# Optimization experiments

Hardware: AMD Instinct MI355X
Metric: run time of the kernel (lower is better)

## Reference

```python
import jax, jax.numpy as jnp
import numpy as np

NUM_GROUPS = 4
EPS = 1e-6


def group_norm(x, scale, bias):
    # x: [b, c, h, w]; GroupNorm32 computes stats in fp32 (x already fp32 here)
    b, c, h, w = x.shape
    xg = x.reshape(b, NUM_GROUPS, c // NUM_GROUPS, h, w)
    mean = jnp.mean(xg, axis=(2, 3, 4), keepdims=True)
    var = jnp.var(xg, axis=(2, 3, 4), keepdims=True)
    xn = ((xg - mean) * jax.lax.rsqrt(var + EPS)).reshape(b, c, h, w)
    return xn * scale[None, :, None, None] + bias[None, :, None, None]


def conv1x1(x, w, b):
    # 1x1 conv == channel mix: x [b,c,h,w], w [co,ci]
    return jnp.einsum('bchw,dc->bdhw', x, w) + b[None, :, None, None]


def setup_inputs() -> dict:
    key = jax.random.key(0)
    ks = jax.random.split(key, 6)
    c = 256
    s = 1.0 / np.sqrt(c)
    return {
        'x': jax.random.normal(ks[0], (4, c, 64, 64), dtype=jnp.float32),
        'gn_scale': jnp.ones((c,), jnp.float32),
        'gn_bias': jnp.zeros((c,), jnp.float32),
        'wq': jax.random.normal(ks[1], (c, c), jnp.float32) * s,
        'bq': jnp.zeros((c,), jnp.float32),
        'wk': jax.random.normal(ks[2], (c, c), jnp.float32) * s,
        'bk': jnp.zeros((c,), jnp.float32),
        'wv': jax.random.normal(ks[3], (c, c), jnp.float32) * s,
        'bv': jnp.zeros((c,), jnp.float32),
        'wproj': jax.random.normal(ks[4], (c, c), jnp.float32) * s,
        'bproj': jnp.zeros((c,), jnp.float32),
    }


def reference(x, gn_scale, gn_bias, wq, bq, wk, bk, wv, bv, wproj, bproj):
    b, c, h, w = x.shape
    hw = h * w
    h_ = group_norm(x, gn_scale, gn_bias)
    q = conv1x1(h_, wq, bq).reshape(b, c, hw)  # [b, c, hw]
    k = conv1x1(h_, wk, bk).reshape(b, c, hw)
    v = conv1x1(h_, wv, bv).reshape(b, c, hw)
    scale = jnp.float32(1.0 / np.sqrt(c))
    # attn[b, i, j] = sum_c q[b,c,i] * k[b,c,j], fp32 softmax over j
    attn = jnp.einsum('bci,bcj->bij', q.astype(jnp.float32), k.astype(jnp.float32)) * scale
    attn = jax.nn.softmax(attn, axis=-1).astype(x.dtype)
    # out[b, c, i] = sum_j v[b,c,j] * attn[b,i,j]
    out = jnp.einsum('bcj,bij->bci', v, attn).reshape(b, c, h, w)
    out = conv1x1(out, wproj, bproj)
    return x + out
```

## Files before the change

### kernel.cpp

```cpp
#include <hip/hip_runtime.h>


#define HW 4096
#define CCH 256
#define NBATCH 4
#define GN_N (64 * HW)

typedef unsigned short u16;
typedef __attribute__((ext_vector_type(8))) short bf16x8;
typedef __attribute__((ext_vector_type(4))) float f32x4;
typedef __attribute__((ext_vector_type(4))) u16 u16x4;

__device__ __forceinline__ u16 f2bf(float f) {
  unsigned u = __float_as_uint(f);
  u += 0x7fffu + ((u >> 16) & 1u);
  return (u16)(u >> 16);
}
__device__ __forceinline__ float bf2f(u16 h) { return __uint_as_float(((unsigned)h) << 16); }

__device__ __forceinline__ void gload_lds16(const void* g, void* l) {
  __builtin_amdgcn_global_load_lds(
      (const __attribute__((address_space(1))) unsigned*)g,
      (__attribute__((address_space(3))) unsigned*)l, 16, 0, 0);
}

__global__ __launch_bounds__(256) void gn_partial(const float* __restrict__ x,
                                                  float* __restrict__ part) {
  const int bg = blockIdx.y, blk = blockIdx.x, tid = threadIdx.x;
  const float4* X = (const float4*)(x + (size_t)bg * GN_N);
  float s = 0.f, ss = 0.f;
#pragma unroll
  for (int u = 0; u < 8; ++u) {
    float4 v = X[blk * 2048 + u * 256 + tid];
    s += v.x + v.y + v.z + v.w;
    ss += v.x * v.x + v.y * v.y + v.z * v.z + v.w * v.w;
  }
  for (int off = 32; off; off >>= 1) { s += __shfl_xor(s, off); ss += __shfl_xor(ss, off); }
  __shared__ float rs[4], rss[4];
  const int w = tid >> 6;
  if ((tid & 63) == 0) { rs[w] = s; rss[w] = ss; }
  __syncthreads();
  if (tid == 0) {
    part[(bg * 32 + blk) * 2 + 0] = rs[0] + rs[1] + rs[2] + rs[3];
    part[(bg * 32 + blk) * 2 + 1] = rss[0] + rss[1] + rss[2] + rss[3];
  }
}

__global__ void gn_finalize(const float* __restrict__ part, float2* __restrict__ stats) {
  const int t = threadIdx.x;
  if (t < 16) {
    float s = 0.f, ss = 0.f;
    for (int u = 0; u < 32; ++u) { s += part[(t * 32 + u) * 2]; ss += part[(t * 32 + u) * 2 + 1]; }
    const float mean = s * (1.0f / GN_N);
    const float var = ss * (1.0f / GN_N) - mean * mean;
    stats[t] = make_float2(mean, rsqrtf(var + 1e-6f));
  }
}

__global__ __launch_bounds__(256) void norm_tr(const float* __restrict__ x,
                                               const float2* __restrict__ stats,
                                               const float* __restrict__ gsc,
                                               const float* __restrict__ gbi,
                                               u16* __restrict__ Ht) {
  __shared__ u16 T[64][72];
  const int i0 = blockIdx.x * 64, c0 = blockIdx.y * 64, b = blockIdx.z;
  const int tid = threadIdx.x;
  const int cl = tid >> 4;
  const int il4 = (tid & 15) * 4;
#pragma unroll
  for (int it = 0; it < 4; ++it) {
    const int c = c0 + it * 16 + cl;
    const float2 st = stats[b * 4 + (c >> 6)];
    const float sc = gsc[c] * st.y;
    const float bi = gbi[c] - st.x * sc;
    const float4 v = *(const float4*)&x[((size_t)(b * CCH + c)) * HW + i0 + il4];
    T[il4 + 0][it * 16 + cl] = f2bf(v.x * sc + bi);
    T[il4 + 1][it * 16 + cl] = f2bf(v.y * sc + bi);
    T[il4 + 2][it * 16 + cl] = f2bf(v.z * sc + bi);
    T[il4 + 3][it * 16 + cl] = f2bf(v.w * sc + bi);
  }
  __syncthreads();
  const int il = tid >> 2, cs = (tid & 3) * 16;
  const uint4 a = *(const uint4*)&T[il][cs];
  const uint4 b2 = *(const uint4*)&T[il][cs + 8];
  const size_t o = ((size_t)b * HW + i0 + il) * CCH + c0 + cs;
  *(uint4*)&Ht[o] = a;
  *(uint4*)&Ht[o + 8] = b2;
}

__global__ __launch_bounds__(256) void wcast(const float* __restrict__ w0, const float* __restrict__ w1,
                                             const float* __restrict__ w2, const float* __restrict__ w3,
                                             u16* __restrict__ dst) {
  const float* src = blockIdx.y == 0 ? w0 : blockIdx.y == 1 ? w1 : blockIdx.y == 2 ? w2 : w3;
  u16* d = dst + (size_t)blockIdx.y * 65536;
  const int idx = (blockIdx.x * 256 + threadIdx.x) * 8;
  const float4 a = *(const float4*)&src[idx];
  const float4 c = *(const float4*)&src[idx + 4];
  uint4 p;
  p.x = (unsigned)f2bf(a.x) | ((unsigned)f2bf(a.y) << 16);
  p.y = (unsigned)f2bf(a.z) | ((unsigned)f2bf(a.w) << 16);
  p.z = (unsigned)f2bf(c.x) | ((unsigned)f2bf(c.y) << 16);
  p.w = (unsigned)f2bf(c.z) | ((unsigned)f2bf(c.w) << 16);
  *(uint4*)&d[idx] = p;
}

template <int EPI, bool HASB>
__global__ __launch_bounds__(256) void gemm2(
    const u16* __restrict__ A, int lda, long sA,
    const u16* __restrict__ Bm, int ldb, long sB,
    void* __restrict__ O0, int ldo, long sO,
    void* __restrict__ O1, void* __restrict__ O2,
    const float* __restrict__ b0, const float* __restrict__ b1, const float* __restrict__ b2,
    const float* __restrict__ aux, long sAux,
    float scale, int K) {
  __shared__ char lsA[32768], lsB[32768];
  int bx, by, bz;
  {
    const int nx = gridDim.x, ny = gridDim.y;
    const int lin = blockIdx.x + nx * (blockIdx.y + ny * blockIdx.z);
    const int q = (nx * ny * (int)gridDim.z) >> 3;
    const int wg = (lin & 7) * q + (lin >> 3);
    bx = wg % nx; const int t2 = wg / nx; by = t2 % ny; bz = t2 / ny;
  }
  const int tid = threadIdx.x;
  const int w = tid >> 6, l = tid & 63;
  const int wm = w >> 1, wn = w & 1;
  const int m0 = by * 128, n0 = bx * 128;
  const u16* Ab = A + (size_t)bz * sA;
  const u16* Bb = Bm + (size_t)bz * sB;

  f32x4 acc[4][4];
#pragma unroll
  for (int i = 0; i < 4; ++i)
#pragma unroll
    for (int j = 0; j < 4; ++j)
#pragma unroll
      for (int q2 = 0; q2 < 4; ++q2) acc[i][j][q2] = 0.f;

  auto stage = [&](int buf, int k0) {
#pragma unroll
    for (int s = 0; s < 4; ++s) {
      const int o = s * 4096 + tid * 16;
      const int r = o >> 7;
      const int c = ((o >> 4) & 7) ^ (r & 7);
      const int ke = c * 8;
      gload_lds16(Ab + (size_t)(m0 + r) * lda + k0 + ke, lsA + buf * 16384 + s * 4096 + w * 1024);
      gload_lds16(Bb + (size_t)(n0 + r) * ldb + k0 + ke, lsB + buf * 16384 + s * 4096 + w * 1024);
    }
  };

  const int nt = K >> 6;
  stage(0, 0);
  asm volatile("s_waitcnt vmcnt(0)" ::: "memory");
  __syncthreads();
  for (int t = 0; t < nt; ++t) {
    const int cur = t & 1;
    if (t + 1 < nt) stage(cur ^ 1, (t + 1) << 6);
#pragma unroll
    for (int kk = 0; kk < 2; ++kk) {
      bf16x8 aF[4], bF[4];
#pragma unroll
      for (int mi = 0; mi < 4; ++mi) {
        const int r = wm * 64 + mi * 16 + (l & 15);
        const int cc = (kk * 4 + (l >> 4)) ^ (r & 7);
        aF[mi] = *(const bf16x8*)(lsA + cur * 16384 + r * 128 + cc * 16);
      }
#pragma unroll
      for (int ni = 0; ni < 4; ++ni) {
        const int r = wn * 64 + ni * 16 + (l & 15);
        const int cc = (kk * 4 + (l >> 4)) ^ (r & 7);
        bF[ni] = *(const bf16x8*)(lsB + cur * 16384 + r * 128 + cc * 16);
      }
#pragma unroll
      for (int mi = 0; mi < 4; ++mi)
#pragma unroll
        for (int ni = 0; ni < 4; ++ni)
          acc[mi][ni] = __builtin_amdgcn_mfma_f32_16x16x32_bf16(aF[mi], bF[ni], acc[mi][ni], 0, 0, 0);
    }
    asm volatile("s_waitcnt vmcnt(0)" ::: "memory");
    __syncthreads();
  }

  const int lc = l & 15;
  const int lr4 = (l >> 4) * 4;

  if (EPI == 5) {
    const int sel = m0 >> 8;
    const float* bs = sel == 0 ? b0 : sel == 1 ? b1 : b2;
#pragma unroll
    for (int mi = 0; mi < 4; ++mi) {
      const int mg = m0 + wm * 64 + mi * 16 + lr4;
      const int mloc = mg & 255;
      const float4 bv = *(const float4*)&bs[mloc];
      float bb4[4] = {bv.x, bv.y, bv.z, bv.w};
#pragma unroll
      for (int ni = 0; ni < 4; ++ni) {
        const int n = n0 + wn * 64 + ni * 16 + lc;
        if (sel == 2) {
          u16* V = (u16*)O2 + (size_t)bz * sO;
#pragma unroll
          for (int q2 = 0; q2 < 4; ++q2) V[(size_t)(mloc + q2) * HW + n] = f2bf(acc[mi][ni][q2] + bb4[q2]);
        } else {
          u16* Oq = (u16*)(sel == 0 ? O0 : O1) + (size_t)bz * sO;
          u16x4 pk;
#pragma unroll
          for (int q2 = 0; q2 < 4; ++q2) pk[q2] = f2bf(acc[mi][ni][q2] + bb4[q2]);
          *(u16x4*)&Oq[(size_t)n * CCH + mloc] = pk;
        }
      }
    }
  } else {
    float* O = (float*)O0 + (size_t)bz * sO;
    const float* R = aux + (size_t)bz * sAux;
#pragma unroll
    for (int mi = 0; mi < 4; ++mi) {
      const int mb = m0 + wm * 64 + mi * 16 + lr4;
      float bb4[4] = {0.f, 0.f, 0.f, 0.f};
      if (HASB) {
        const float4 bv = *(const float4*)&b0[mb];
        bb4[0] = bv.x; bb4[1] = bv.y; bb4[2] = bv.z; bb4[3] = bv.w;
      }
#pragma unroll
      for (int ni = 0; ni < 4; ++ni) {
        const int n = n0 + wn * 64 + ni * 16 + lc;
#pragma unroll
        for (int q2 = 0; q2 < 4; ++q2)
          O[(size_t)(mb + q2) * ldo + n] = acc[mi][ni][q2] * scale + bb4[q2] + R[(size_t)(mb + q2) * ldo + n];
      }
    }
  }
}

#define LBUF 65664
__global__ __launch_bounds__(512, 2) void attn_fused(
    const u16* __restrict__ Qt, const u16* __restrict__ Kt, const u16* __restrict__ Vv,
    float* __restrict__ Opart, float* __restrict__ Rpart) {
  __shared__ __attribute__((aligned(16))) char lds[2 * LBUF];
  __shared__ __attribute__((aligned(16))) unsigned P_lds[8][16][36];
  const int bid = blockIdx.x;
  const int g8 = bid & 7, it = bid >> 3;
  const int b = g8 >> 1, jh = g8 & 1;
  const int tid = threadIdx.x, w = tid >> 6, l = tid & 63;
  const int g = l >> 4, base = l & 15;
  const u16* Qb = Qt + (size_t)b * HW * CCH;
  const u16* Kb = Kt + (size_t)b * HW * CCH;
  const u16* Vb = Vv + (size_t)b * CCH * HW;
  const int iw0 = it * 128 + w * 16;

  bf16x8 q[8];
#pragma unroll
  for (int kc = 0; kc < 8; ++kc)
    q[kc] = *(const bf16x8*)&Qb[(size_t)(iw0 + base) * CCH + kc * 32 + g * 8];

  f32x4 oacc[16];
#pragma unroll
  for (int nc = 0; nc < 16; ++nc)
#pragma unroll
    for (int r = 0; r < 4; ++r) oacc[nc][r] = 0.f;
  float rsum = 0.f;

  auto stage = [&](int buf, int j0) {
    char* Kl = lds + buf * LBUF;
    char* Vl = Kl + 32768;
#pragma unroll
    for (int s = 0; s < 8; ++s) {
      const int i = w * 8 + s;
      if (i < 32) {
        const int row = i * 2 + (l >> 5);
        const int c5 = l & 31;
        gload_lds16(Kb + (size_t)(j0 + row) * CCH + ((c5 ^ (row & 7)) * 8), Kl + i * 1024);
      } else {
        const int jj = i - 32;
        const int jg = jj >> 2;
        const int cc = (jj & 3) * 64 + l;
        gload_lds16(Vb + (size_t)cc * HW + j0 + jg * 8, Vl + jg * 4112 + (jj & 3) * 1024);
      }
    }
  };

  const int j0base = jh * 2048;
  const int NT = 32;
  stage(0, j0base);
  asm volatile("s_waitcnt vmcnt(0)" ::: "memory");
  __syncthreads();

  for (int t = 0; t < NT; ++t) {
    const int cur = t & 1;
    if (t + 1 < NT) stage(cur ^ 1, j0base + (t + 1) * 64);
    const char* Kl = lds + cur * LBUF;
    const char* Vl = Kl + 32768;
    f32x4 sacc[4];
#pragma unroll
    for (int mj = 0; mj < 4; ++mj)
#pragma unroll
      for (int r = 0; r < 4; ++r) sacc[mj][r] = 0.f;
#pragma unroll
    for (int kc = 0; kc < 8; ++kc) {
      bf16x8 kf[4];
#pragma unroll
      for (int mj = 0; mj < 4; ++mj) {
        const int row = mj * 16 + base;
        const int c5 = (kc * 4 + g) ^ (row & 7);
        kf[mj] = *(const bf16x8*)(Kl + row * 512 + c5 * 16);
      }
#pragma unroll
      for (int mj = 0; mj < 4; ++mj)
        sacc[mj] = __builtin_amdgcn_mfma_f32_16x16x32_bf16(kf[mj], q[kc], sacc[mj], 0, 0, 0);
    }
#pragma unroll
    for (int mj = 0; mj < 4; ++mj) {
      const float p0 = __expf(sacc[mj][0] * 0.0625f - 8.0f);
      const float p1 = __expf(sacc[mj][1] * 0.0625f - 8.0f);
      const float p2 = __expf(sacc[mj][2] * 0.0625f - 8.0f);
      const float p3 = __expf(sacc[mj][3] * 0.0625f - 8.0f);
      const u16 e0 = f2bf(p0), e1 = f2bf(p1), e2 = f2bf(p2), e3 = f2bf(p3);
      rsum += (bf2f(e0) + bf2f(e1)) + (bf2f(e2) + bf2f(e3));
      P_lds[w][base][mj * 8 + g * 2 + 0] = (unsigned)e0 | ((unsigned)e1 << 16);
      P_lds[w][base][mj * 8 + g * 2 + 1] = (unsigned)e2 | ((unsigned)e3 << 16);
    }
    asm volatile("s_waitcnt lgkmcnt(0)" ::: "memory");
    __builtin_amdgcn_sched_barrier(0);
    bf16x8 af[2];
#pragma unroll
    for (int ks = 0; ks < 2; ++ks)
      af[ks] = *(const bf16x8*)&P_lds[w][base][ks * 16 + g * 4];
#pragma unroll
    for (int nc = 0; nc < 16; ++nc) {
#pragma unroll
      for (int ks = 0; ks < 2; ++ks) {
        const bf16x8 vf = *(const bf16x8*)(Vl + (ks * 4 + g) * 4112 + (nc * 16 + base) * 16);
        oacc[nc] = __builtin_amdgcn_mfma_f32_16x16x32_bf16(af[ks], vf, oacc[nc], 0, 0, 0);
      }
    }
    asm volatile("s_waitcnt vmcnt(0)" ::: "memory");
    __syncthreads();
  }

  rsum += __shfl_xor(rsum, 16);
  rsum += __shfl_xor(rsum, 32);
  if (l < 16) Rpart[(size_t)jh * 16384 + b * HW + iw0 + l] = rsum;
  float* Op = Opart + (size_t)jh * 16384 * CCH + (size_t)b * HW * CCH;
#pragma unroll
  for (int nc = 0; nc < 16; ++nc) {
    const int c = nc * 16 + base;
#pragma unroll
    for (int r = 0; r < 4; ++r) {
      const int row = iw0 + g * 4 + r;
      Op[(size_t)row * CCH + c] = oacc[nc][r];
    }
  }
}

__global__ __launch_bounds__(256) void attn_combine(const float* __restrict__ Op,
                                                    const float* __restrict__ Rp,
                                                    u16* __restrict__ Ot) {
  const int idx = blockIdx.x * 256 + threadIdx.x;
  const int row = idx >> 6;
  const int c4 = (idx & 63) * 4;
  const float4 o0 = *(const float4*)&Op[(size_t)row * CCH + c4];
  const float4 o1 = *(const float4*)&Op[(size_t)16384 * CCH + (size_t)row * CCH + c4];
  const float inv = 1.0f / (Rp[row] + Rp[16384 + row]);
  u16x4 r;
  r[0] = f2bf((o0.x + o1.x) * inv);
  r[1] = f2bf((o0.y + o1.y) * inv);
  r[2] = f2bf((o0.z + o1.z) * inv);
  r[3] = f2bf((o0.w + o1.w) * inv);
  *(u16x4*)&Ot[(size_t)row * CCH + c4] = r;
}

extern "C" void kernel_launch(void* const* d_in, const int* in_sizes, int n_in,
                              void* d_out, int out_size, void* d_ws, size_t ws_size,
                              hipStream_t stream) {
  const float* x   = (const float*)d_in[0];
  const float* gsc = (const float*)d_in[1];
  const float* gbi = (const float*)d_in[2];
  const float* wq  = (const float*)d_in[3];
  const float* bq  = (const float*)d_in[4];
  const float* wk  = (const float*)d_in[5];
  const float* bk  = (const float*)d_in[6];
  const float* wv  = (const float*)d_in[7];
  const float* bv  = (const float*)d_in[8];
  const float* wp  = (const float*)d_in[9];
  const float* bp  = (const float*)d_in[10];
  float* out = (float*)d_out;

  char* ws = (char*)d_ws;
  size_t off = 0;
  auto alloc = [&](size_t bytes) {
    size_t o = off; off = (off + bytes + 255) & ~(size_t)255; return o;
  };
  const size_t szMat = (size_t)NBATCH * HW * CCH * 2;
  u16* W      = (u16*)(ws + alloc(4 * 65536 * 2));
  float* pgn  = (float*)(ws + alloc(16 * 32 * 2 * 4));
  float2* st  = (float2*)(ws + alloc(16 * 8));
  u16* Ht = (u16*)(ws + alloc(szMat));
  u16* Qt = (u16*)(ws + alloc(szMat));
  u16* Kt = (u16*)(ws + alloc(szMat));
  u16* Vv = (u16*)(ws + alloc(szMat));
  u16* Ot = (u16*)(ws + alloc(szMat));
  float* Opart = (float*)(ws + alloc((size_t)2 * 16384 * CCH * 4));
  float* Rpart = (float*)(ws + alloc((size_t)2 * 16384 * 4));

  const long sM = (long)HW * CCH;

  wcast<<<dim3(32, 4), 256, 0, stream>>>(wq, wk, wv, wp, W);
  gn_partial<<<dim3(32, 16), 256, 0, stream>>>(x, pgn);
  gn_finalize<<<1, 64, 0, stream>>>(pgn, st);
  norm_tr<<<dim3(HW / 64, CCH / 64, NBATCH), 256, 0, stream>>>(x, st, gsc, gbi, Ht);

  gemm2<5, true><<<dim3(32, 6, NBATCH), 256, 0, stream>>>(
      W, 256, 0, Ht, 256, sM, Qt, 256, sM, Kt, Vv, bq, bk, bv, nullptr, 0, 1.f, 256);

  attn_fused<<<256, 512, 0, stream>>>(Qt, Kt, Vv, Opart, Rpart);
  attn_combine<<<4096, 256, 0, stream>>>(Opart, Rpart, Ot);

  gemm2<2, true><<<dim3(32, 2, NBATCH), 256, 0, stream>>>(
      W + 3 * 65536, 256, 0, Ot, 256, sM, out, HW, (long)CCH * HW, nullptr, nullptr,
      bp, nullptr, nullptr, x, (long)CCH * HW, 1.f, 256);
}
```

Before: 156.9 us.

## Restructure fused attention into 256-thread blocks with shared P tile and channel-split PV

The attention kernel drops from 512-thread blocks with 128 query rows to 256-thread blocks with 64 query rows, doubling the grid to 512 blocks. Each key tile shrinks to 32 keys, so there are twice as many iterations. In the PV stage each wave now reads the whole block's P tile from shared LDS and owns a 64-channel slice of V, rather than one private 16-row P against all channels. The goal is less V fragment traffic per wave and more blocks for occupancy. In exchange it adds an extra barrier per iteration, halves the K/V staging per step, and sets s_setprio around the MFMA sections.

```diff
diff --git a/kernel.cpp b/kernel.cpp
--- a/kernel.cpp
+++ b/kernel.cpp
@@ -231,122 +231,130 @@
   }
 }
 
-#define LBUF 65664
-__global__ __launch_bounds__(512, 2) void attn_fused(
+#define LBUFA 32768
+__global__ __launch_bounds__(256) void attn_fused(
     const u16* __restrict__ Qt, const u16* __restrict__ Kt, const u16* __restrict__ Vv,
     float* __restrict__ Opart, float* __restrict__ Rpart) {
-  __shared__ __attribute__((aligned(16))) char lds[2 * LBUF];
-  __shared__ __attribute__((aligned(16))) unsigned P_lds[8][16][36];
+  __shared__ __attribute__((aligned(16))) char lds[2 * LBUFA];
+  __shared__ __attribute__((aligned(16))) unsigned P_block[64][20];
   const int bid = blockIdx.x;
-  const int g8 = bid & 7, it = bid >> 3;
-  const int b = g8 >> 1, jh = g8 & 1;
+  const int it = bid >> 3, b = (bid >> 1) & 3, jh = bid & 1;
   const int tid = threadIdx.x, w = tid >> 6, l = tid & 63;
   const int g = l >> 4, base = l & 15;
   const u16* Qb = Qt + (size_t)b * HW * CCH;
   const u16* Kb = Kt + (size_t)b * HW * CCH;
   const u16* Vb = Vv + (size_t)b * CCH * HW;
-  const int iw0 = it * 128 + w * 16;
+  const int iw0 = it * 64 + w * 16;
 
   bf16x8 q[8];
 #pragma unroll
   for (int kc = 0; kc < 8; ++kc)
     q[kc] = *(const bf16x8*)&Qb[(size_t)(iw0 + base) * CCH + kc * 32 + g * 8];
 
-  f32x4 oacc[16];
-#pragma unroll
-  for (int nc = 0; nc < 16; ++nc)
-#pragma unroll
-    for (int r = 0; r < 4; ++r) oacc[nc][r] = 0.f;
+  f32x4 oacc[4][4];
+#pragma unroll
+  for (int fi = 0; fi < 4; ++fi)
+#pragma unroll
+    for (int cf = 0; cf < 4; ++cf)
+#pragma unroll
+      for (int r = 0; r < 4; ++r) oacc[fi][cf][r] = 0.f;
   float rsum = 0.f;
 
   auto stage = [&](int buf, int j0) {
-    char* Kl = lds + buf * LBUF;
-    char* Vl = Kl + 32768;
+    char* Kl = lds + buf * LBUFA;
+    char* Vl = Kl + 16384;
 #pragma unroll
     for (int s = 0; s < 8; ++s) {
-      const int i = w * 8 + s;
-      if (i < 32) {
+      const int i = s * 4 + w;
+      if (i < 16) {
         const int row = i * 2 + (l >> 5);
         const int c5 = l & 31;
         gload_lds16(Kb + (size_t)(j0 + row) * CCH + ((c5 ^ (row & 7)) * 8), Kl + i * 1024);
       } else {
-        const int jj = i - 32;
-        const int jg = jj >> 2;
-        const int cc = (jj & 3) * 64 + l;
-        gload_lds16(Vb + (size_t)cc * HW + j0 + jg * 8, Vl + jg * 4112 + (jj & 3) * 1024);
+        const int jj = i - 16;
+        const int jg = jj >> 2, sub = jj & 3;
+        const int cc = sub * 64 + l;
+        gload_lds16(Vb + (size_t)cc * HW + j0 + jg * 8, Vl + jg * 4096 + sub * 1024);
       }
     }
   };
 
   const int j0base = jh * 2048;
-  const int NT = 32;
+  const int NT = 64;
   stage(0, j0base);
   asm volatile("s_waitcnt vmcnt(0)" ::: "memory");
-  __syncthreads();
+  __builtin_amdgcn_s_barrier();
 
   for (int t = 0; t < NT; ++t) {
     const int cur = t & 1;
-    if (t + 1 < NT) stage(cur ^ 1, j0base + (t + 1) * 64);
-    const char* Kl = lds + cur * LBUF;
-    const char* Vl = Kl + 32768;
-    f32x4 sacc[4];
-#pragma unroll
-    for (int mj = 0; mj < 4; ++mj)
+    if (t + 1 < NT) stage(cur ^ 1, j0base + (t + 1) * 32);
+    const char* Kl = lds + cur * LBUFA;
+    const char* Vl = Kl + 16384;
+    f32x4 sacc[2];
+#pragma unroll
+    for (int mj = 0; mj < 2; ++mj)
 #pragma unroll
       for (int r = 0; r < 4; ++r) sacc[mj][r] = 0.f;
+    __builtin_amdgcn_s_setprio(1);
 #pragma unroll
     for (int kc = 0; kc < 8; ++kc) {
-      bf16x8 kf[4];
-#pragma unroll
-      for (int mj = 0; mj < 4; ++mj) {
+      bf16x8 kf[2];
+#pragma unroll
+      for (int mj = 0; mj < 2; ++mj) {
         const int row = mj * 16 + base;
         const int c5 = (kc * 4 + g) ^ (row & 7);
         kf[mj] = *(const bf16x8*)(Kl + row * 512 + c5 * 16);
       }
 #pragma unroll
-      for (int mj = 0; mj < 4; ++mj)
+      for (int mj = 0; mj < 2; ++mj)
         sacc[mj] = __builtin_amdgcn_mfma_f32_16x16x32_bf16(kf[mj], q[kc], sacc[mj], 0, 0, 0);
     }
-#pragma unroll
-    for (int mj = 0; mj < 4; ++mj) {
+    __builtin_amdgcn_s_setprio(0);
+    const int iL = w * 16 + base;
+#pragma unroll
+    for (int mj = 0; mj < 2; ++mj) {
       const float p0 = __expf(sacc[mj][0] * 0.0625f - 8.0f);
       const float p1 = __expf(sacc[mj][1] * 0.0625f - 8.0f);
       const float p2 = __expf(sacc[mj][2] * 0.0625f - 8.0f);
       const float p3 = __expf(sacc[mj][3] * 0.0625f - 8.0f);
       const u16 e0 = f2bf(p0), e1 = f2bf(p1), e2 = f2bf(p2), e3 = f2bf(p3);
       rsum += (bf2f(e0) + bf2f(e1)) + (bf2f(e2) + bf2f(e3));
-      P_lds[w][base][mj * 8 + g * 2 + 0] = (unsigned)e0 | ((unsigned)e1 << 16);
-      P_lds[w][base][mj * 8 + g * 2 + 1] = (unsigned)e2 | ((unsigned)e3 << 16);
+      P_block[iL][mj * 8 + g * 2 + 0] = (unsigned)e0 | ((unsigned)e1 << 16);
+      P_block[iL][mj * 8 + g * 2 + 1] = (unsigned)e2 | ((unsigned)e3 << 16);
     }
     asm volatile("s_waitcnt lgkmcnt(0)" ::: "memory");
     __builtin_amdgcn_sched_barrier(0);
-    bf16x8 af[2];
-#pragma unroll
-    for (int ks = 0; ks < 2; ++ks)
-      af[ks] = *(const bf16x8*)&P_lds[w][base][ks * 16 + g * 4];
-#pragma unroll
-    for (int nc = 0; nc < 16; ++nc) {
-#pragma unroll
-      for (int ks = 0; ks < 2; ++ks) {
-        const bf16x8 vf = *(const bf16x8*)(Vl + (ks * 4 + g) * 4112 + (nc * 16 + base) * 16);
-        oacc[nc] = __builtin_amdgcn_mfma_f32_16x16x32_bf16(af[ks], vf, oacc[nc], 0, 0, 0);
-      }
-    }
-    asm volatile("s_waitcnt vmcnt(0)" ::: "memory");
-    __syncthreads();
+    __builtin_amdgcn_s_barrier();
+    bf16x8 vf[4];
+#pragma unroll
+    for (int cf = 0; cf < 4; ++cf)
+      vf[cf] = *(const bf16x8*)(Vl + g * 4096 + (w * 64 + cf * 16 + base) * 16);
+    __builtin_amdgcn_s_setprio(1);
+#pragma unroll
+    for (int fi = 0; fi < 4; ++fi) {
+      const bf16x8 af = *(const bf16x8*)&P_block[fi * 16 + base][g * 4];
+#pragma unroll
+      for (int cf = 0; cf < 4; ++cf)
+        oacc[fi][cf] = __builtin_amdgcn_mfma_f32_16x16x32_bf16(af, vf[cf], oacc[fi][cf], 0, 0, 0);
+    }
+    __builtin_amdgcn_s_setprio(0);
+    asm volatile("s_waitcnt vmcnt(0) lgkmcnt(0)" ::: "memory");
+    __builtin_amdgcn_sched_barrier(0);
+    __builtin_amdgcn_s_barrier();
   }
 
   rsum += __shfl_xor(rsum, 16);
   rsum += __shfl_xor(rsum, 32);
   if (l < 16) Rpart[(size_t)jh * 16384 + b * HW + iw0 + l] = rsum;
-  float* Op = Opart + (size_t)jh * 16384 * CCH + (size_t)b * HW * CCH;
-#pragma unroll
-  for (int nc = 0; nc < 16; ++nc) {
-    const int c = nc * 16 + base;
-#pragma unroll
-    for (int r = 0; r < 4; ++r) {
-      const int row = iw0 + g * 4 + r;
-      Op[(size_t)row * CCH + c] = oacc[nc][r];
+  float* Op = Opart + (size_t)jh * 16384 * CCH + (size_t)b * HW * CCH + (size_t)it * 64 * CCH;
+#pragma unroll
+  for (int fi = 0; fi < 4; ++fi) {
+#pragma unroll
+    for (int cf = 0; cf < 4; ++cf) {
+      const int c = w * 64 + cf * 16 + base;
+#pragma unroll
+      for (int r = 0; r < 4; ++r)
+        Op[(size_t)(fi * 16 + g * 4 + r) * CCH + c] = oacc[fi][cf][r];
     }
   }
 }
@@ -411,7 +419,7 @@
   gemm2<5, true><<<dim3(32, 6, NBATCH), 256, 0, stream>>>(
       W, 256, 0, Ht, 256, sM, Qt, 256, sM, Kt, Vv, bq, bk, bv, nullptr, 0, 1.f, 256);
 
-  attn_fused<<<256, 512, 0, stream>>>(Qt, Kt, Vv, Opart, Rpart);
+  attn_fused<<<512, 256, 0, stream>>>(Qt, Kt, Vv, Opart, Rpart);
   attn_combine<<<4096, 256, 0, stream>>>(Opart, Rpart, Ot);
 
   gemm2<2, true><<<dim3(32, 2, NBATCH), 256, 0, stream>>>(
```

Measured after the change: 187.7 us. 1.2x slower.
